# Optimization experiments

Hardware: AMD Instinct MI355X
Metric: run time of the kernel (lower is better)

## Reference

```python
import jax, jax.numpy as jnp
import numpy as np

NHEADS = 64; EMB = 2048; STATE = 128; KCONV = 4; NGROUPS = 1
HEAD_DIM = 64; CHUNK = 128; EPS = 1e-6
INTER = NHEADS * HEAD_DIM                  # int(expand*emb_dim) = 4096
CONV_DIM = INTER + 2 * NGROUPS * STATE     # 4352
PROJ = INTER + CONV_DIM + NHEADS           # 8512
BATCH = 2; SEQ = 2048


def segsum(x):
    # x: (..., T) -> (..., T, T) stable segment sums; -inf strictly above diagonal
    T = x.shape[-1]
    xe = jnp.broadcast_to(x[..., None], x.shape + (T,))
    m_strict = jnp.tril(jnp.ones((T, T), bool), -1)
    s = jnp.cumsum(jnp.where(m_strict, xe, 0.0), axis=-2)
    m_incl = jnp.tril(jnp.ones((T, T), bool), 0)
    return jnp.where(m_incl, s, -jnp.inf)


def setup_inputs() -> dict:
    key = jax.random.key(0)
    ks = jax.random.split(key, 6)
    x = jax.random.normal(ks[0], (BATCH, SEQ, EMB), jnp.float32)
    in_proj_w = jax.random.normal(ks[1], (PROJ, EMB), jnp.float32) * 0.02
    conv_w = jax.random.normal(ks[2], (CONV_DIM, 1, KCONV), jnp.float32) * 0.2
    conv_b = jax.random.normal(ks[3], (CONV_DIM,), jnp.float32) * 0.1
    dt_bias = jnp.ones((NHEADS,), jnp.float32)
    A_log = jnp.log(jnp.arange(1, NHEADS + 1, dtype=jnp.float32))
    D = jnp.ones((NHEADS,), jnp.float32)
    norm_w = jnp.ones((INTER,), jnp.float32)
    out_proj_w = jax.random.normal(ks[4], (EMB, INTER), jnp.float32) * 0.02
    mask = jnp.ones((BATCH, 1, SEQ), jnp.int32)  # shape[1]==1 -> masking is a no-op, as in torch path
    return {"x": x, "in_proj_w": in_proj_w, "conv_w": conv_w, "conv_b": conv_b,
            "dt_bias": dt_bias, "A_log": A_log, "D": D, "norm_w": norm_w,
            "out_proj_w": out_proj_w, "mask": mask}


def reference(x, in_proj_w, conv_w, conv_b, dt_bias, A_log, D, norm_w, out_proj_w, mask):
    b, s, _ = x.shape
    proj = x @ in_proj_w.T                                    # (b,s,PROJ)
    gate = proj[..., :INTER]
    hBC = proj[..., INTER:INTER + CONV_DIM]
    dt = proj[..., INTER + CONV_DIM:]                         # (b,s,H)

    # causal depthwise conv1d (torch pads k-1 both sides then truncates to seq_len == left-pad k-1)
    conv = jax.lax.conv_general_dilated(
        hBC.transpose(0, 2, 1), conv_w, (1,), [(KCONV - 1, 0)],
        feature_group_count=CONV_DIM)
    hBC = jax.nn.silu((conv + conv_b[None, :, None]).transpose(0, 2, 1))

    hid = hBC[..., :INTER]
    Bm = hBC[..., INTER:INTER + NGROUPS * STATE]
    Cm = hBC[..., INTER + NGROUPS * STATE:]

    A = -jnp.exp(A_log)                                       # (H,)
    dt = jax.nn.softplus(dt + dt_bias)                        # clamp(0,inf) is a no-op after softplus

    hid = hid.reshape(b, s, NHEADS, HEAD_DIM)
    pad = (CHUNK - s % CHUNK) % CHUNK
    D_res = D[:, None] * jnp.pad(hid, ((0, 0), (0, pad), (0, 0), (0, 0)))
    hid = hid * dt[..., None]
    A_s = A * dt                                              # (b,s,H)
    Bm = jnp.tile(Bm.reshape(b, s, NGROUPS, STATE), (1, 1, NHEADS // NGROUPS, 1))
    Cm = jnp.tile(Cm.reshape(b, s, NGROUPS, STATE), (1, 1, NHEADS // NGROUPS, 1))

    def chunkify(t):
        t = jnp.pad(t, ((0, 0), (0, pad)) + ((0, 0),) * (t.ndim - 2))
        return t.reshape(b, -1, CHUNK, *t.shape[2:])

    hid_c, A_c, B_c, C_c = (chunkify(t) for t in (hid, A_s, Bm, Cm))
    A_c = A_c.transpose(0, 3, 1, 2)                           # (b,H,c,l)
    A_cum = jnp.cumsum(A_c, -1)

    # intra-chunk (diagonal blocks)
    L = jnp.exp(segsum(A_c))                                  # (b,H,c,l,l)
    G = jnp.einsum('bclhn,bcshn->bhcls', C_c, B_c)
    Y_diag = jnp.einsum('bhcls,bcshp->bclhp', G * L, hid_c)

    # per-chunk end states
    decay_states = jnp.exp(A_cum[..., -1:] - A_cum)           # (b,H,c,l)
    states = jnp.einsum('bclhn,bhcl,bclhp->bchpn', B_c, decay_states, hid_c)

    # inter-chunk recurrence
    A_last = jnp.pad(A_cum[..., -1], ((0, 0), (0, 0), (1, 0)))  # (b,H,c+1)
    decay_chunk = jnp.exp(segsum(A_last))                     # (b,H,c+1,c+1)
    states = jnp.concatenate([jnp.zeros_like(states[:, :1]), states], axis=1)
    new_states = jnp.einsum('bhzc,bchpn->bzhpn', decay_chunk, states)
    states = new_states[:, :-1]                               # states entering each chunk

    # off-diagonal (cross-chunk) contribution
    state_decay = jnp.exp(A_cum)                              # (b,H,c,l)
    Y_off = jnp.einsum('bclhn,bchpn,bhcl->bclhp', C_c, states, state_decay)

    y = (Y_diag + Y_off).reshape(b, -1, NHEADS, HEAD_DIM) + D_res
    y = y[:, :s].reshape(b, s, INTER)

    # gated RMSNorm
    yg = y * jax.nn.silu(gate)
    yn = norm_w * (yg * jax.lax.rsqrt(jnp.mean(yg * yg, -1, keepdims=True) + EPS))
    return yn @ out_proj_w.T
```

## Files before the change

### kernel.cpp

```cpp
#include <hip/hip_runtime.h>
#include <math.h>

#define NHEADS   64
#define EMB      2048
#define STATE    128
#define KCONV    4
#define HEAD_DIM 64
#define CHUNK    128
#define SEQL     2048
#define NBATCH   2
#define NCH      (SEQL/CHUNK)
#define INTER    (NHEADS*HEAD_DIM)
#define CONVD    (INTER + 2*STATE)
#define PROJD    (INTER + CONVD + NHEADS)
#define ROWS     (NBATCH*SEQL)
#define EPSV     1e-6f

__device__ __forceinline__ float sigmoidf_(float x){ return 1.f/(1.f+__expf(-x)); }

__device__ __forceinline__ float b2f(ushort u){
  union{float f; unsigned u;} x; x.u = ((unsigned)u)<<16; return x.f;
}
__device__ __forceinline__ ushort f2b(float f){
  union{float f; unsigned u;} x; x.f=f;
  unsigned r = x.u + 0x7FFFu + ((x.u>>16)&1u);
  return (ushort)(r>>16);
}
__device__ __forceinline__ float4 ld4(const float* p){ return *(const float4*)p; }
__device__ __forceinline__ float4 ld4(const ushort* p){
  ushort4 v = *(const ushort4*)p;
  return make_float4(b2f(v.x),b2f(v.y),b2f(v.z),b2f(v.w));
}
__device__ __forceinline__ void st4(float* p, float4 v){ *(float4*)p = v; }
__device__ __forceinline__ void st4(ushort* p, float4 v){
  ushort4 o; o.x=f2b(v.x); o.y=f2b(v.y); o.z=f2b(v.z); o.w=f2b(v.w);
  *(ushort4*)p = o;
}
__device__ __forceinline__ void stc(float* p, float v){ *p = v; }
__device__ __forceinline__ void stc(ushort* p, float v){ *p = f2b(v); }

__global__ __launch_bounds__(256) void f32_to_bf16_kernel(
    const float* __restrict__ in, ushort* __restrict__ out, long n)
{
  long i = ((long)blockIdx.x*256 + threadIdx.x) * 8;
  if (i >= n) return;
  float4 a = *(const float4*)(in + i);
  float4 b = *(const float4*)(in + i + 4);
  st4(out + i, a);
  st4(out + i + 4, b);
}

typedef __attribute__((ext_vector_type(8))) short short8v;
typedef __attribute__((ext_vector_type(4))) float float4v;

#define GLL16(g, l) __builtin_amdgcn_global_load_lds( \
    (const __attribute__((address_space(1))) void*)(g), \
    (__attribute__((address_space(3))) void*)(l), 16, 0, 0)

template<typename TC>
__global__ __launch_bounds__(256) void gemm_mfma_bt(
    const ushort* __restrict__ A, int lda,
    const ushort* __restrict__ B, int ldb,
    TC* __restrict__ C, int ldc,
    int N, int K)
{
  __shared__ ushort As[128*32];
  __shared__ ushort Bs[128*32];
  const int t = threadIdx.x;
  const int lt = t & 63, w = t >> 6;
  const int wr = w >> 1, wc = w & 1;

  const int nwg = gridDim.x * gridDim.y;
  int orig = blockIdx.x + gridDim.x * blockIdx.y;
  int tile = orig;
  if ((nwg & 7) == 0) tile = (orig & 7) * (nwg >> 3) + (orig >> 3);
  const int m0 = (tile / gridDim.x) * 128;
  const int n0 = (tile % gridDim.x) * 128;

  float4v acc[4][4];
  #pragma unroll
  for (int i=0;i<4;++i)
    #pragma unroll
    for (int j=0;j<4;++j) acc[i][j] = float4v{0.f,0.f,0.f,0.f};

  const int srow = t >> 2;
  const int scol = (t & 3) * 8;
  const int bn0 = min(n0 + srow, N-1);
  const int bn1 = min(n0 + 64 + srow, N-1);
  const long aoff0 = (long)(m0 + srow) * lda + scol;
  const long aoff1 = (long)(m0 + 64 + srow) * lda + scol;
  const long boff0 = (long)bn0 * ldb + scol;
  const long boff1 = (long)bn1 * ldb + scol;
  const int lr = lt & 15, lk = (lt >> 4) * 8;

  for (int k0 = 0; k0 < K; k0 += 32) {
    GLL16(A + aoff0 + k0, As + t*8);
    GLL16(A + aoff1 + k0, As + 2048 + t*8);
    GLL16(B + boff0 + k0, Bs + t*8);
    GLL16(B + boff1 + k0, Bs + 2048 + t*8);
    __syncthreads();
    short8v af[4], bf[4];
    #pragma unroll
    for (int i = 0; i < 4; ++i) {
      af[i] = *(const short8v*)(As + (wr*64 + i*16 + lr)*32 + lk);
      bf[i] = *(const short8v*)(Bs + (wc*64 + i*16 + lr)*32 + lk);
    }
    #pragma unroll
    for (int i = 0; i < 4; ++i)
      #pragma unroll
      for (int j = 0; j < 4; ++j)
        acc[i][j] = __builtin_amdgcn_mfma_f32_16x16x32_bf16(af[i], bf[j], acc[i][j], 0, 0, 0);
    __syncthreads();
  }

  const int cr = (lt >> 4) * 4;
  const int cc = lt & 15;
  #pragma unroll
  for (int i = 0; i < 4; ++i) {
    #pragma unroll
    for (int j = 0; j < 4; ++j) {
      int col = n0 + wc*64 + j*16 + cc;
      if (col < N) {
        #pragma unroll
        for (int r = 0; r < 4; ++r) {
          int row = m0 + wr*64 + i*16 + cr + r;
          stc(C + (long)row*ldc + col, acc[i][j][r]);
        }
      }
    }
  }
}

#define BM 128
#define BN 128
#define BKK 16

template<typename TA, typename TB, typename TC>
__global__ __launch_bounds__(256) void gemm_bnt(
    const TA* __restrict__ A, int lda, long sA,
    const TB* __restrict__ B, int ldb, long sB,
    TC* __restrict__ C, int ldc, long sC,
    int M, int N, int K)
{
  A += (long)blockIdx.z * sA;
  B += (long)blockIdx.z * sB;
  C += (long)blockIdx.z * sC;
  const int n0 = blockIdx.x * BN;
  const int m0 = blockIdx.y * BM;
  __shared__ float As[BKK][BM+4];
  __shared__ float Bs[BKK][BN+4];
  const int t = threadIdx.x;
  const int tx = t & 15, ty = t >> 4;
  float acc[8][8];
  #pragma unroll
  for (int i=0;i<8;++i)
    #pragma unroll
    for (int j=0;j<8;++j) acc[i][j]=0.f;

  for (int k0 = 0; k0 < K; k0 += BKK) {
    #pragma unroll
    for (int i = 0; i < 2; ++i) {
      int f = t + i*256;
      int row = f >> 2, kq = (f & 3) << 2;
      float4 v = ld4(A + (long)(m0+row)*lda + (k0 + kq));
      As[kq+0][row]=v.x; As[kq+1][row]=v.y; As[kq+2][row]=v.z; As[kq+3][row]=v.w;
      int gn = n0 + row;
      float4 w = make_float4(0.f,0.f,0.f,0.f);
      if (gn < N) w = ld4(B + (long)gn*ldb + (k0 + kq));
      Bs[kq+0][row]=w.x; Bs[kq+1][row]=w.y; Bs[kq+2][row]=w.z; Bs[kq+3][row]=w.w;
    }
    __syncthreads();
    #pragma unroll
    for (int k = 0; k < BKK; ++k) {
      float a[8], b[8];
      *(float4*)&a[0] = *(const float4*)&As[k][ty*8];
      *(float4*)&a[4] = *(const float4*)&As[k][ty*8+4];
      *(float4*)&b[0] = *(const float4*)&Bs[k][tx*8];
      *(float4*)&b[4] = *(const float4*)&Bs[k][tx*8+4];
      #pragma unroll
      for (int i = 0; i < 8; ++i)
        #pragma unroll
        for (int j = 0; j < 8; ++j)
          acc[i][j] = fmaf(a[i], b[j], acc[i][j]);
    }
    __syncthreads();
  }
  #pragma unroll
  for (int i = 0; i < 8; ++i) {
    int gm = m0 + ty*8 + i;
    #pragma unroll
    for (int j = 0; j < 8; j += 4) {
      int gn = n0 + tx*8 + j;
      if (gn < N)
        st4(C + (long)gm*ldc + gn,
            make_float4(acc[i][j],acc[i][j+1],acc[i][j+2],acc[i][j+3]));
    }
  }
}

__global__ __launch_bounds__(256) void conv_silu_kernel(
    const ushort* __restrict__ proj, const float* __restrict__ cw,
    const float* __restrict__ cb, ushort* __restrict__ out)
{
  const int C4 = CONVD/4;
  long idx = (long)blockIdx.x*256 + threadIdx.x;
  if (idx >= (long)ROWS*C4) return;
  int r = (int)(idx / C4);
  int c = (int)(idx % C4) * 4;
  int tt = r & (SEQL-1);
  float4 bv = *(const float4*)(cb + c);
  float acc0=bv.x, acc1=bv.y, acc2=bv.z, acc3=bv.w;
  float4 w0 = *(const float4*)(cw + (c+0)*KCONV);
  float4 w1 = *(const float4*)(cw + (c+1)*KCONV);
  float4 w2 = *(const float4*)(cw + (c+2)*KCONV);
  float4 w3 = *(const float4*)(cw + (c+3)*KCONV);
  const float wj0[4] = {w0.x,w0.y,w0.z,w0.w};
  const float wj1[4] = {w1.x,w1.y,w1.z,w1.w};
  const float wj2[4] = {w2.x,w2.y,w2.z,w2.w};
  const float wj3[4] = {w3.x,w3.y,w3.z,w3.w};
  #pragma unroll
  for (int j = 0; j < KCONV; ++j) {
    int tr = tt - (KCONV-1) + j;
    if (tr >= 0) {
      float4 v = ld4(proj + (long)(r - (KCONV-1) + j)*PROJD + INTER + c);
      acc0 = fmaf(v.x, wj0[j], acc0);
      acc1 = fmaf(v.y, wj1[j], acc1);
      acc2 = fmaf(v.z, wj2[j], acc2);
      acc3 = fmaf(v.w, wj3[j], acc3);
    }
  }
  float4 o;
  o.x = acc0 * sigmoidf_(acc0);
  o.y = acc1 * sigmoidf_(acc1);
  o.z = acc2 * sigmoidf_(acc2);
  o.w = acc3 * sigmoidf_(acc3);
  st4(out + (long)r*CONVD + c, o);
}

__global__ void dt_kernel(const ushort* __restrict__ proj,
                          const float* __restrict__ dt_bias,
                          float* __restrict__ dtb)
{
  int idx = blockIdx.x*256 + threadIdx.x;
  if (idx >= ROWS*NHEADS) return;
  int r = idx >> 6, h = idx & 63;
  float xv = b2f(proj[(long)r*PROJD + INTER + CONVD + h]) + dt_bias[h];
  dtb[idx] = fmaxf(xv, 0.f) + __logf(1.f + __expf(-fabsf(xv)));
}

__global__ void acum_kernel(const float* __restrict__ dtb,
                            const float* __restrict__ A_log,
                            float* __restrict__ acum)
{
  int idx = blockIdx.x*256 + threadIdx.x;
  if (idx >= NBATCH*NCH*NHEADS) return;
  int h = idx & 63, bc = idx >> 6;
  float Ah = -__expf(A_log[h]);
  const float* d = dtb + (long)bc*CHUNK*NHEADS + h;
  float* o = acum + (long)idx*CHUNK;
  float acc = 0.f;
  for (int l = 0; l < CHUNK; ++l) { acc = fmaf(Ah, d[l*NHEADS], acc); o[l] = acc; }
}

__global__ __launch_bounds__(256) void states_mfma_kernel(
    const ushort* __restrict__ conv, const float* __restrict__ dtb,
    const float* __restrict__ acum, ushort* __restrict__ states)
{
  const int h = blockIdx.x, c = blockIdx.y, b = blockIdx.z;
  const int bc = b*NCH + c;
  const long r0 = (long)bc*CHUNK;
  __shared__ ushort Ahi[64][136];
  __shared__ ushort Alo[64][136];
  __shared__ ushort Bt[128][136];
  __shared__ float arow[CHUNK];
  __shared__ float wrow[CHUNK];
  const int t = threadIdx.x;
  const int lt = t & 63, w = t >> 6;
  const int lr = lt & 15, lk = (lt >> 4) * 8;

  if (t < CHUNK) arow[t] = acum[((long)bc*NHEADS + h)*CHUNK + t];
  __syncthreads();
  if (t < CHUNK) wrow[t] = dtb[(r0 + t)*NHEADS + h] * __expf(arow[CHUNK-1] - arow[t]);
  __syncthreads();

  for (int i = t; i < CHUNK*HEAD_DIM/8; i += 256) {
    int l = i >> 3, p0 = (i & 7) * 8;
    short8v v = *(const short8v*)(conv + (r0+l)*CONVD + h*HEAD_DIM + p0);
    float wl = wrow[l];
    #pragma unroll
    for (int j = 0; j < 8; ++j) {
      float f = b2f((ushort)v[j]) * wl;
      ushort hb = f2b(f);
      Ahi[p0+j][l] = hb;
      Alo[p0+j][l] = f2b(f - b2f(hb));
    }
  }
  for (int i = t; i < CHUNK*STATE/8; i += 256) {
    int l = i >> 4, n0 = (i & 15) * 8;
    short8v v = *(const short8v*)(conv + (r0+l)*CONVD + INTER + n0);
    #pragma unroll
    for (int j = 0; j < 8; ++j) Bt[n0+j][l] = (ushort)v[j];
  }
  __syncthreads();

  float4v acc[8];
  #pragma unroll
  for (int j = 0; j < 8; ++j) acc[j] = float4v{0,0,0,0};
  #pragma unroll
  for (int kk = 0; kk < 4; ++kk) {
    short8v ahi = *(const short8v*)&Ahi[w*16 + lr][kk*32 + lk];
    short8v alo = *(const short8v*)&Alo[w*16 + lr][kk*32 + lk];
    #pragma unroll
    for (int nj = 0; nj < 8; ++nj) {
      short8v bv = *(const short8v*)&Bt[nj*16 + lr][kk*32 + lk];
      acc[nj] = __builtin_amdgcn_mfma_f32_16x16x32_bf16(ahi, bv, acc[nj], 0, 0, 0);
      acc[nj] = __builtin_amdgcn_mfma_f32_16x16x32_bf16(alo, bv, acc[nj], 0, 0, 0);
    }
  }
  ushort* so = states + ((long)bc*NHEADS + h)*HEAD_DIM*STATE;
  const int cr = (lt >> 4) * 4, cc = lt & 15;
  #pragma unroll
  for (int nj = 0; nj < 8; ++nj)
    #pragma unroll
    for (int r = 0; r < 4; ++r)
      so[(w*16 + cr + r)*STATE + nj*16 + cc] = f2b(acc[nj][r]);
}

__global__ __launch_bounds__(256) void scan_kernel(
    ushort* __restrict__ states, const float* __restrict__ acum)
{
  const int bh = blockIdx.x;
  const int b = bh >> 6, h = bh & 63;
  const int t = threadIdx.x;
  float acc[32];
  #pragma unroll
  for (int i=0;i<32;++i) acc[i]=0.f;
  for (int c = 0; c < NCH; ++c) {
    const long bch = ((long)(b*NCH + c)*NHEADS + h);
    float lam = __expf(acum[bch*CHUNK + CHUNK-1]);
    ushort* sb = states + bch*HEAD_DIM*STATE;
    #pragma unroll
    for (int i = 0; i < 32; ++i) {
      float v = b2f(sb[t + i*256]);
      sb[t + i*256] = f2b(acc[i]);
      acc[i] = fmaf(acc[i], lam, v);
    }
  }
}

__global__ __launch_bounds__(256) void y_mfma_kernel(
    const ushort* __restrict__ conv, const float* __restrict__ dtb,
    const float* __restrict__ acum, const float* __restrict__ G,
    const ushort* __restrict__ states, const float* __restrict__ Dp,
    ushort* __restrict__ proj)
{
  const int h = blockIdx.x;
  const int c = blockIdx.y >> 1, mh = blockIdx.y & 1;
  const int b = blockIdx.z;
  const int bc = b*NCH + c;
  const int mbase = mh * 64;
  const long r0 = (long)bc*CHUNK;

  __shared__ float  Af[64][132];
  __shared__ ushort B0[64][136];
  __shared__ ushort B1[64][136];
  __shared__ float arow[CHUNK];
  __shared__ float dtr[CHUNK];
  __shared__ float el[64];

  const int t = threadIdx.x;
  const int lt = t & 63, w = t >> 6;
  const int lr = lt & 15, lk = (lt >> 4) * 8;

  if (t < CHUNK) {
    arow[t] = acum[((long)bc*NHEADS + h)*CHUNK + t];
    dtr[t]  = dtb[(r0 + t)*NHEADS + h];
  }
  __syncthreads();

  if (t < 64) el[t] = __expf(arow[mbase + t]);
  for (int i = t; i < CHUNK*HEAD_DIM/8; i += 256) {
    int s = i >> 3, p0 = (i & 7) * 8;
    short8v v = *(const short8v*)(conv + (r0+s)*CONVD + h*HEAD_DIM + p0);
    #pragma unroll
    for (int j = 0; j < 8; ++j) B0[p0+j][s] = (ushort)v[j];
  }
  {
    const ushort* stb = states + ((long)bc*NHEADS + h)*HEAD_DIM*STATE;
    for (int i = t; i < HEAD_DIM*STATE/8; i += 256) {
      int p = i >> 4, n0 = (i & 15) * 8;
      *(short8v*)&B1[p][n0] = *(const short8v*)(stb + p*STATE + n0);
    }
  }
  {
    const float* Gb = G + (long)bc*CHUNK*CHUNK;
    for (int i = t; i < 64*CHUNK; i += 256) {
      int ll = i >> 7, s = i & 127;
      int l = mbase + ll;
      float wv = 0.f;
      if (s <= l) wv = Gb[l*CHUNK + s] * __expf(arow[l] - arow[s]) * dtr[s];
      Af[ll][s] = wv;
    }
  }
  __syncthreads();

  float4v acc1[4], acc2[4];
  #pragma unroll
  for (int j = 0; j < 4; ++j) { acc1[j] = float4v{0,0,0,0}; acc2[j] = float4v{0,0,0,0}; }

  #pragma unroll
  for (int kk = 0; kk < 4; ++kk) {
    const float* ap = &Af[w*16 + lr][kk*32 + lk];
    float a8[8];
    *(float4*)&a8[0] = *(const float4*)ap;
    *(float4*)&a8[4] = *(const float4*)(ap + 4);
    short8v ahi, alo;
    #pragma unroll
    for (int e = 0; e < 8; ++e) {
      ushort hb = f2b(a8[e]);
      float rem = a8[e] - b2f(hb);
      ahi[e] = (short)hb;
      alo[e] = (short)f2b(rem);
    }
    #pragma unroll
    for (int nj = 0; nj < 4; ++nj) {
      short8v bfv = *(const short8v*)&B0[nj*16 + lr][kk*32 + lk];
      acc1[nj] = __builtin_amdgcn_mfma_f32_16x16x32_bf16(ahi, bfv, acc1[nj], 0, 0, 0);
      acc1[nj] = __builtin_amdgcn_mfma_f32_16x16x32_bf16(alo, bfv, acc1[nj], 0, 0, 0);
    }
  }
  __syncthreads();

  for (int i = t; i < 64*STATE; i += 256) {
    int ll = i >> 7, n = i & 127;
    Af[ll][n] = b2f(conv[(r0 + mbase + ll)*CONVD + INTER + STATE + n]);
  }
  __syncthreads();

  #pragma unroll
  for (int kk = 0; kk < 4; ++kk) {
    const float* ap = &Af[w*16 + lr][kk*32 + lk];
    float a8[8];
    *(float4*)&a8[0] = *(const float4*)ap;
    *(float4*)&a8[4] = *(const float4*)(ap + 4);
    short8v ahi;
    #pragma unroll
    for (int e = 0; e < 8; ++e) ahi[e] = (short)f2b(a8[e]);
    #pragma unroll
    for (int nj = 0; nj < 4; ++nj) {
      short8v bfv = *(const short8v*)&B1[nj*16 + lr][kk*32 + lk];
      acc2[nj] = __builtin_amdgcn_mfma_f32_16x16x32_bf16(ahi, bfv, acc2[nj], 0, 0, 0);
    }
  }

  const float Dh = Dp[h];
  const int cr = (lt >> 4) * 4, cc = lt & 15;
  #pragma unroll
  for (int nj = 0; nj < 4; ++nj) {
    int p = nj*16 + cc;
    #pragma unroll
    for (int r = 0; r < 4; ++r) {
      int ll = w*16 + cr + r;
      float hid_raw = b2f(B0[p][mbase + ll]);
      float yv = acc1[nj][r] + el[ll]*acc2[nj][r] + Dh*hid_raw;
      proj[(r0 + mbase + ll)*PROJD + INTER + h*HEAD_DIM + p] = f2b(yv);
    }
  }
}

__global__ __launch_bounds__(256) void gate_norm_kernel(
    ushort* __restrict__ proj, const float* __restrict__ nw)
{
  const int r = blockIdx.x;
  const int t = threadIdx.x;
  __shared__ float red[256];
  ushort* gate = proj + (long)r*PROJD;
  ushort* y = gate + INTER;
  float vals[16];
  float ss = 0.f;
  #pragma unroll
  for (int k = 0; k < 4; ++k) {
    int j = (t + k*256) * 4;
    float4 g = ld4(gate + j);
    float4 yv = ld4(y + j);
    float v0 = yv.x * g.x * sigmoidf_(g.x);
    float v1 = yv.y * g.y * sigmoidf_(g.y);
    float v2 = yv.z * g.z * sigmoidf_(g.z);
    float v3 = yv.w * g.w * sigmoidf_(g.w);
    vals[k*4+0]=v0; vals[k*4+1]=v1; vals[k*4+2]=v2; vals[k*4+3]=v3;
    ss += v0*v0 + v1*v1 + v2*v2 + v3*v3;
  }
  red[t] = ss;
  __syncthreads();
  for (int sft = 128; sft > 0; sft >>= 1) {
    if (t < sft) red[t] += red[t+sft];
    __syncthreads();
  }
  float scale = rsqrtf(red[0] / (float)INTER + EPSV);
  #pragma unroll
  for (int k = 0; k < 4; ++k) {
    int j = (t + k*256) * 4;
    float4 w = *(const float4*)(nw + j);
    st4(y + j, make_float4(vals[k*4+0]*scale*w.x, vals[k*4+1]*scale*w.y,
                           vals[k*4+2]*scale*w.z, vals[k*4+3]*scale*w.w));
  }
}

extern "C" void kernel_launch(void* const* d_in, const int* in_sizes, int n_in,
                              void* d_out, int out_size, void* d_ws, size_t ws_size,
                              hipStream_t stream) {
  const float* x       = (const float*)d_in[0];
  const float* Wi      = (const float*)d_in[1];
  const float* cw      = (const float*)d_in[2];
  const float* cb      = (const float*)d_in[3];
  const float* dt_bias = (const float*)d_in[4];
  const float* A_log   = (const float*)d_in[5];
  const float* Dp      = (const float*)d_in[6];
  const float* nw      = (const float*)d_in[7];
  const float* Wo      = (const float*)d_in[8];
  float* out = (float*)d_out;

  ushort* projb = (ushort*)d_ws;
  ushort* R     = projb + (size_t)ROWS*PROJD;
  ushort* xb    = R;
  ushort* Wib   = R + (size_t)ROWS*EMB;
  ushort* Wob   = R;
  ushort* convb = R;
  float*  dtb   = (float*)(convb + (size_t)ROWS*CONVD);
  float*  acum  = dtb  + (size_t)ROWS*NHEADS;
  float*  Gb    = acum + (size_t)NBATCH*NCH*NHEADS*CHUNK;
  ushort* st    = (ushort*)(Gb + (size_t)NBATCH*NCH*CHUNK*CHUNK);

  size_t need = (size_t)ROWS*PROJD*2 + (size_t)ROWS*CONVD*2
              + (size_t)ROWS*NHEADS*4 + (size_t)NBATCH*NCH*NHEADS*CHUNK*4
              + (size_t)NBATCH*NCH*CHUNK*CHUNK*4
              + (size_t)NBATCH*NCH*NHEADS*HEAD_DIM*STATE*2;
  if (ws_size < need) return;

  f32_to_bf16_kernel<<<(int)((long)ROWS*EMB/8/256), 256, 0, stream>>>(x, xb, (long)ROWS*EMB);
  f32_to_bf16_kernel<<<(int)((long)PROJD*EMB/8/256), 256, 0, stream>>>(Wi, Wib, (long)PROJD*EMB);
  gemm_mfma_bt<ushort><<<dim3((PROJD+127)/128, ROWS/128), 256, 0, stream>>>(
      xb, EMB, Wib, EMB, projb, PROJD, PROJD, EMB);
  conv_silu_kernel<<<(int)(((long)ROWS*(CONVD/4)+255)/256), 256, 0, stream>>>(
      projb, cw, cb, convb);
  dt_kernel<<<ROWS*NHEADS/256, 256, 0, stream>>>(projb, dt_bias, dtb);
  acum_kernel<<<(NBATCH*NCH*NHEADS+255)/256, 256, 0, stream>>>(dtb, A_log, acum);
  gemm_bnt<ushort,ushort,float><<<dim3(1,1,NBATCH*NCH), 256, 0, stream>>>(
      convb + INTER + STATE, CONVD, (long)CHUNK*CONVD,
      convb + INTER,         CONVD, (long)CHUNK*CONVD,
      Gb, CHUNK, (long)CHUNK*CHUNK, CHUNK, CHUNK, CHUNK);
  states_mfma_kernel<<<dim3(NHEADS, NCH, NBATCH), 256, 0, stream>>>(convb, dtb, acum, st);
  scan_kernel<<<NBATCH*NHEADS, 256, 0, stream>>>(st, acum);
  y_mfma_kernel<<<dim3(NHEADS, NCH*2, NBATCH), 256, 0, stream>>>(
      convb, dtb, acum, Gb, st, Dp, projb);
  gate_norm_kernel<<<ROWS, 256, 0, stream>>>(projb, nw);
  f32_to_bf16_kernel<<<(int)((long)EMB*INTER/8/256), 256, 0, stream>>>(Wo, Wob, (long)EMB*INTER);
  gemm_mfma_bt<float><<<dim3(EMB/128, ROWS/128), 256, 0, stream>>>(
      projb + INTER, PROJD, Wob, INTER, out, EMB, EMB, INTER);
}
```

Baseline: 661.8 us.

## Swizzle GEMM LDS tiles, use MFMA for C·Bᵀ, fuse dt/cumsum, split scan

```diff
diff --git a/kernel.cpp b/kernel.cpp
--- a/kernel.cpp
+++ b/kernel.cpp
@@ -84,14 +84,14 @@
     for (int j=0;j<4;++j) acc[i][j] = float4v{0.f,0.f,0.f,0.f};
 
   const int srow = t >> 2;
-  const int scol = (t & 3) * 8;
+  const int scol = ((t & 3) ^ ((srow >> 1) & 3)) * 8;
   const int bn0 = min(n0 + srow, N-1);
   const int bn1 = min(n0 + 64 + srow, N-1);
   const long aoff0 = (long)(m0 + srow) * lda + scol;
   const long aoff1 = (long)(m0 + 64 + srow) * lda + scol;
   const long boff0 = (long)bn0 * ldb + scol;
   const long boff1 = (long)bn1 * ldb + scol;
-  const int lr = lt & 15, lk = (lt >> 4) * 8;
+  const int lr = lt & 15, lks = lt >> 4;
 
   for (int k0 = 0; k0 < K; k0 += 32) {
     GLL16(A + aoff0 + k0, As + t*8);
@@ -102,8 +102,10 @@
     short8v af[4], bf[4];
     #pragma unroll
     for (int i = 0; i < 4; ++i) {
-      af[i] = *(const short8v*)(As + (wr*64 + i*16 + lr)*32 + lk);
-      bf[i] = *(const short8v*)(Bs + (wc*64 + i*16 + lr)*32 + lk);
+      int ra = wr*64 + i*16 + lr;
+      af[i] = *(const short8v*)(As + ra*32 + ((lks ^ ((ra>>1)&3)) << 3));
+      int rb = wc*64 + i*16 + lr;
+      bf[i] = *(const short8v*)(Bs + rb*32 + ((lks ^ ((rb>>1)&3)) << 3));
     }
     #pragma unroll
     for (int i = 0; i < 4; ++i)
@@ -131,71 +133,49 @@
   }
 }
 
-#define BM 128
-#define BN 128
-#define BKK 16
-
-template<typename TA, typename TB, typename TC>
-__global__ __launch_bounds__(256) void gemm_bnt(
-    const TA* __restrict__ A, int lda, long sA,
-    const TB* __restrict__ B, int ldb, long sB,
-    TC* __restrict__ C, int ldc, long sC,
-    int M, int N, int K)
-{
-  A += (long)blockIdx.z * sA;
-  B += (long)blockIdx.z * sB;
-  C += (long)blockIdx.z * sC;
-  const int n0 = blockIdx.x * BN;
-  const int m0 = blockIdx.y * BM;
-  __shared__ float As[BKK][BM+4];
-  __shared__ float Bs[BKK][BN+4];
-  const int t = threadIdx.x;
-  const int tx = t & 15, ty = t >> 4;
-  float acc[8][8];
-  #pragma unroll
-  for (int i=0;i<8;++i)
-    #pragma unroll
-    for (int j=0;j<8;++j) acc[i][j]=0.f;
-
-  for (int k0 = 0; k0 < K; k0 += BKK) {
-    #pragma unroll
-    for (int i = 0; i < 2; ++i) {
-      int f = t + i*256;
-      int row = f >> 2, kq = (f & 3) << 2;
-      float4 v = ld4(A + (long)(m0+row)*lda + (k0 + kq));
-      As[kq+0][row]=v.x; As[kq+1][row]=v.y; As[kq+2][row]=v.z; As[kq+3][row]=v.w;
-      int gn = n0 + row;
-      float4 w = make_float4(0.f,0.f,0.f,0.f);
-      if (gn < N) w = ld4(B + (long)gn*ldb + (k0 + kq));
-      Bs[kq+0][row]=w.x; Bs[kq+1][row]=w.y; Bs[kq+2][row]=w.z; Bs[kq+3][row]=w.w;
-    }
-    __syncthreads();
-    #pragma unroll
-    for (int k = 0; k < BKK; ++k) {
-      float a[8], b[8];
-      *(float4*)&a[0] = *(const float4*)&As[k][ty*8];
-      *(float4*)&a[4] = *(const float4*)&As[k][ty*8+4];
-      *(float4*)&b[0] = *(const float4*)&Bs[k][tx*8];
-      *(float4*)&b[4] = *(const float4*)&Bs[k][tx*8+4];
+__global__ __launch_bounds__(256) void g_mfma_kernel(
+    const ushort* __restrict__ conv, float* __restrict__ G)
+{
+  const int bc = blockIdx.x;
+  const long r0 = (long)bc*CHUNK;
+  __shared__ ushort Cs[128][136];
+  __shared__ ushort Bs[128][136];
+  const int t = threadIdx.x;
+  const int lt = t & 63, w = t >> 6;
+  const int lr = lt & 15, lk = (lt >> 4) * 8;
+
+  for (int i = t; i < 128*16; i += 256) {
+    int r = i >> 4, n0 = (i & 15) * 8;
+    *(short8v*)&Cs[r][n0] = *(const short8v*)(conv + (r0+r)*CONVD + INTER + STATE + n0);
+    *(short8v*)&Bs[r][n0] = *(const short8v*)(conv + (r0+r)*CONVD + INTER + n0);
+  }
+  __syncthreads();
+
+  float4v acc[2][8];
+  #pragma unroll
+  for (int m=0;m<2;++m)
+    #pragma unroll
+    for (int j=0;j<8;++j) acc[m][j] = float4v{0,0,0,0};
+  #pragma unroll
+  for (int kk = 0; kk < 4; ++kk) {
+    short8v a0 = *(const short8v*)&Cs[w*32 +      lr][kk*32 + lk];
+    short8v a1 = *(const short8v*)&Cs[w*32 + 16 + lr][kk*32 + lk];
+    #pragma unroll
+    for (int nj = 0; nj < 8; ++nj) {
+      short8v bv = *(const short8v*)&Bs[nj*16 + lr][kk*32 + lk];
+      acc[0][nj] = __builtin_amdgcn_mfma_f32_16x16x32_bf16(a0, bv, acc[0][nj], 0, 0, 0);
+      acc[1][nj] = __builtin_amdgcn_mfma_f32_16x16x32_bf16(a1, bv, acc[1][nj], 0, 0, 0);
+    }
+  }
+  float* Gb = G + (long)bc*CHUNK*CHUNK;
+  const int cr = (lt >> 4) * 4, cc = lt & 15;
+  #pragma unroll
+  for (int m = 0; m < 2; ++m)
+    #pragma unroll
+    for (int nj = 0; nj < 8; ++nj)
       #pragma unroll
-      for (int i = 0; i < 8; ++i)
-        #pragma unroll
-        for (int j = 0; j < 8; ++j)
-          acc[i][j] = fmaf(a[i], b[j], acc[i][j]);
-    }
-    __syncthreads();
-  }
-  #pragma unroll
-  for (int i = 0; i < 8; ++i) {
-    int gm = m0 + ty*8 + i;
-    #pragma unroll
-    for (int j = 0; j < 8; j += 4) {
-      int gn = n0 + tx*8 + j;
-      if (gn < N)
-        st4(C + (long)gm*ldc + gn,
-            make_float4(acc[i][j],acc[i][j+1],acc[i][j+2],acc[i][j+3]));
-    }
-  }
+      for (int r = 0; r < 4; ++r)
+        Gb[(w*32 + m*16 + cr + r)*CHUNK + nj*16 + cc] = acc[m][nj][r];
 }
 
 __global__ __launch_bounds__(256) void conv_silu_kernel(
@@ -237,29 +217,33 @@
   st4(out + (long)r*CONVD + c, o);
 }
 
-__global__ void dt_kernel(const ushort* __restrict__ proj,
-                          const float* __restrict__ dt_bias,
-                          float* __restrict__ dtb)
-{
-  int idx = blockIdx.x*256 + threadIdx.x;
-  if (idx >= ROWS*NHEADS) return;
-  int r = idx >> 6, h = idx & 63;
-  float xv = b2f(proj[(long)r*PROJD + INTER + CONVD + h]) + dt_bias[h];
-  dtb[idx] = fmaxf(xv, 0.f) + __logf(1.f + __expf(-fabsf(xv)));
-}
-
-__global__ void acum_kernel(const float* __restrict__ dtb,
-                            const float* __restrict__ A_log,
-                            float* __restrict__ acum)
-{
-  int idx = blockIdx.x*256 + threadIdx.x;
-  if (idx >= NBATCH*NCH*NHEADS) return;
-  int h = idx & 63, bc = idx >> 6;
-  float Ah = -__expf(A_log[h]);
-  const float* d = dtb + (long)bc*CHUNK*NHEADS + h;
-  float* o = acum + (long)idx*CHUNK;
-  float acc = 0.f;
-  for (int l = 0; l < CHUNK; ++l) { acc = fmaf(Ah, d[l*NHEADS], acc); o[l] = acc; }
+__global__ __launch_bounds__(256) void dt_acum_kernel(
+    const ushort* __restrict__ proj, const float* __restrict__ dt_bias,
+    const float* __restrict__ A_log, float* __restrict__ dtb,
+    float* __restrict__ acum)
+{
+  const int bc = blockIdx.x;
+  const long r0 = (long)bc*CHUNK;
+  __shared__ float dts[CHUNK][NHEADS+1];
+  const int t = threadIdx.x;
+  for (int i = t; i < CHUNK*8; i += 256) {
+    int l = i >> 3, h0 = (i & 7) * 8;
+    short8v v = *(const short8v*)(proj + (r0+l)*PROJD + INTER + CONVD + h0);
+    #pragma unroll
+    for (int j = 0; j < 8; ++j) {
+      float xv = b2f((ushort)v[j]) + dt_bias[h0+j];
+      float sp = fmaxf(xv, 0.f) + __logf(1.f + __expf(-fabsf(xv)));
+      dts[l][h0+j] = sp;
+      dtb[(r0+l)*NHEADS + h0 + j] = sp;
+    }
+  }
+  __syncthreads();
+  if (t < NHEADS) {
+    float Ah = -__expf(A_log[t]);
+    float acc = 0.f;
+    float* o = acum + ((long)bc*NHEADS + t)*CHUNK;
+    for (int l = 0; l < CHUNK; ++l) { acc = fmaf(Ah, dts[l][t], acc); o[l] = acc; }
+  }
 }
 
 __global__ __launch_bounds__(256) void states_mfma_kernel(
@@ -329,18 +313,20 @@
 __global__ __launch_bounds__(256) void scan_kernel(
     ushort* __restrict__ states, const float* __restrict__ acum)
 {
-  const int bh = blockIdx.x;
+  const int blk = blockIdx.x;
+  const int bh = blk >> 2, pq = blk & 3;
   const int b = bh >> 6, h = bh & 63;
   const int t = threadIdx.x;
-  float acc[32];
-  #pragma unroll
-  for (int i=0;i<32;++i) acc[i]=0.f;
+  const int base = pq * 16 * STATE;
+  float acc[8];
+  #pragma unroll
+  for (int i=0;i<8;++i) acc[i]=0.f;
   for (int c = 0; c < NCH; ++c) {
     const long bch = ((long)(b*NCH + c)*NHEADS + h);
     float lam = __expf(acum[bch*CHUNK + CHUNK-1]);
-    ushort* sb = states + bch*HEAD_DIM*STATE;
-    #pragma unroll
-    for (int i = 0; i < 32; ++i) {
+    ushort* sb = states + bch*HEAD_DIM*STATE + base;
+    #pragma unroll
+    for (int i = 0; i < 8; ++i) {
       float v = b2f(sb[t + i*256]);
       sb[t + i*256] = f2b(acc[i]);
       acc[i] = fmaf(acc[i], lam, v);
@@ -543,14 +529,10 @@
       xb, EMB, Wib, EMB, projb, PROJD, PROJD, EMB);
   conv_silu_kernel<<<(int)(((long)ROWS*(CONVD/4)+255)/256), 256, 0, stream>>>(
       projb, cw, cb, convb);
-  dt_kernel<<<ROWS*NHEADS/256, 256, 0, stream>>>(projb, dt_bias, dtb);
-  acum_kernel<<<(NBATCH*NCH*NHEADS+255)/256, 256, 0, stream>>>(dtb, A_log, acum);
-  gemm_bnt<ushort,ushort,float><<<dim3(1,1,NBATCH*NCH), 256, 0, stream>>>(
-      convb + INTER + STATE, CONVD, (long)CHUNK*CONVD,
-      convb + INTER,         CONVD, (long)CHUNK*CONVD,
-      Gb, CHUNK, (long)CHUNK*CHUNK, CHUNK, CHUNK, CHUNK);
+  dt_acum_kernel<<<NBATCH*NCH, 256, 0, stream>>>(projb, dt_bias, A_log, dtb, acum);
+  g_mfma_kernel<<<NBATCH*NCH, 256, 0, stream>>>(convb, Gb);
   states_mfma_kernel<<<dim3(NHEADS, NCH, NBATCH), 256, 0, stream>>>(convb, dtb, acum, st);
-  scan_kernel<<<NBATCH*NHEADS, 256, 0, stream>>>(st, acum);
+  scan_kernel<<<NBATCH*NHEADS*4, 256, 0, stream>>>(st, acum);
   y_mfma_kernel<<<dim3(NHEADS, NCH*2, NBATCH), 256, 0, stream>>>(
       convb, dtb, acum, Gb, st, Dp, projb);
   gate_norm_kernel<<<ROWS, 256, 0, stream>>>(projb, nw);
```

Result: faster. 619.0 us (-6.5%).
